# Optimization experiments

Hardware: AMD Instinct MI355X
Metric: run time of the kernel (lower is better)

## Reference

```python
import jax, jax.numpy as jnp
import numpy as np

B, S, H, NH = 2, 2048, 1024, 16
DK = H // NH

def setup_inputs() -> dict:
    key = jax.random.key(0)
    ks = jax.random.split(key, 8)
    scale = 0.02
    return {
        "x": jax.random.normal(ks[0], (B, S, H), jnp.float32),
        "mask": jax.random.randint(ks[1], (B, S, S), 0, 2, jnp.int32),
        "alibi": jax.random.normal(ks[2], (1, NH, S, S), jnp.float32),
        "W_q": jax.random.normal(ks[3], (H, H), jnp.float32) * scale,
        "b_q": jnp.zeros((H,), jnp.float32),
        "W_k": jax.random.normal(ks[4], (H, H), jnp.float32) * scale,
        "b_k": jnp.zeros((H,), jnp.float32),
        "W_v": jax.random.normal(ks[5], (H, H), jnp.float32) * scale,
        "b_v": jnp.zeros((H,), jnp.float32),
        "W_o": jax.random.normal(ks[6], (H, H), jnp.float32) * scale,
        "b_o": jnp.zeros((H,), jnp.float32),
    }

def reference(x, mask, alibi, W_q, b_q, W_k, b_k, W_v, b_v, W_o, b_o):
    b, s, h = x.shape
    def split_heads(t):  # [B,S,H] -> [B,NH,S,DK]
        return t.reshape(b, s, NH, DK).transpose(0, 2, 1, 3)
    q = split_heads(x @ W_q + b_q)
    k = split_heads(x @ W_k + b_k)
    v = split_heads(x @ W_v + b_v)
    scores = jnp.einsum("bhqd,bhkd->bhqk", q, k) / jnp.sqrt(jnp.float32(DK))
    scores = scores + alibi
    scores = jnp.where(mask[:, None, :, :] == 0, jnp.float32(-1e9), scores)
    probs = jax.nn.softmax(scores, axis=-1)  # dropout is identity in eval
    ctx = jnp.einsum("bhqk,bhkd->bhqd", probs, v)
    ctx = ctx.transpose(0, 2, 1, 3).reshape(b, s, h)
    return ctx @ W_o + b_o
```

## Files before the change

kernel.cpp:

```cpp
#include <hip/hip_runtime.h>
#include <hip/hip_bf16.h>


#define S_LEN 2048
#define H_DIM 1024
#define N_HEADS 16

typedef __bf16 bf16x8 __attribute__((ext_vector_type(8)));
typedef __bf16 bf16x4 __attribute__((ext_vector_type(4)));
typedef float f32x4 __attribute__((ext_vector_type(4)));

using gvoid = __attribute__((address_space(1))) void;
using svoid = __attribute__((address_space(3))) void;

static __device__ __forceinline__ f32x4 mfma16(bf16x8 a, bf16x8 b, f32x4 c) {
  return __builtin_amdgcn_mfma_f32_16x16x32_bf16(a, b, c, 0, 0, 0);
}

template <int NCH, int NW>
static __device__ __forceinline__ void stage64(const __bf16* g, int rstride,
                                               __bf16* lds, int wid, int lane) {
#pragma unroll
  for (int i = 0; i < NCH / NW; ++i) {
    int chunk = i * NW + wid;
    int u = chunk * 64 + lane;
    int r = u >> 3, s = u & 7;
    const __bf16* src = g + (size_t)r * rstride + ((s ^ (r & 7)) << 3);
    __builtin_amdgcn_global_load_lds((const gvoid*)src,
                                     (svoid*)(lds + chunk * 512), 16, 0, 0);
  }
}

static __device__ __forceinline__ bf16x8 read_frag(const __bf16* lds, int r,
                                                   int slot) {
  return *(const bf16x8*)(lds + r * 64 + ((slot ^ (r & 7)) << 3));
}

__global__ __launch_bounds__(256) void k_convert_x(const float* __restrict__ x,
                                                   __bf16* __restrict__ xb) {
  size_t idx = ((size_t)blockIdx.x * 256 + threadIdx.x) * 8;
  float4 a = *(const float4*)(x + idx);
  float4 b = *(const float4*)(x + idx + 4);
  bf16x8 o;
  o[0] = (__bf16)a.x; o[1] = (__bf16)a.y; o[2] = (__bf16)a.z; o[3] = (__bf16)a.w;
  o[4] = (__bf16)b.x; o[5] = (__bf16)b.y; o[6] = (__bf16)b.z; o[7] = (__bf16)b.w;
  *(bf16x8*)(xb + idx) = o;
}

__global__ __launch_bounds__(256) void k_transpose_w(
    const float* __restrict__ w0, const float* __restrict__ w1,
    const float* __restrict__ w2, const float* __restrict__ w3,
    __bf16* __restrict__ wt) {
  __shared__ float t[64][65];
  int z = blockIdx.z;
  const float* W = (z == 0) ? w0 : (z == 1) ? w1 : (z == 2) ? w2 : w3;
  __bf16* O = wt + (size_t)z * H_DIM * H_DIM;
  int k0 = blockIdx.x * 64, n0 = blockIdx.y * 64;
  int tid = threadIdx.x;
  {
    int r = tid >> 4, c4 = tid & 15;
#pragma unroll
    for (int i = 0; i < 4; ++i) {
      float4 v = *(const float4*)(W + (size_t)(k0 + r + i * 16) * H_DIM + n0 + c4 * 4);
      t[r + i * 16][c4 * 4 + 0] = v.x;
      t[r + i * 16][c4 * 4 + 1] = v.y;
      t[r + i * 16][c4 * 4 + 2] = v.z;
      t[r + i * 16][c4 * 4 + 3] = v.w;
    }
  }
  __syncthreads();
  {
    int nn = tid >> 2, js = (tid & 3) * 16;
    bf16x8 o0, o1;
#pragma unroll
    for (int j = 0; j < 8; ++j) {
      o0[j] = (__bf16)t[js + j][nn];
      o1[j] = (__bf16)t[js + 8 + j][nn];
    }
    __bf16* dst = O + (size_t)(n0 + nn) * H_DIM + k0 + js;
    *(bf16x8*)dst = o0;
    *(bf16x8*)(dst + 8) = o1;
  }
}

__global__ __launch_bounds__(256) void k_transpose_v(const __bf16* __restrict__ V,
                                                     __bf16* __restrict__ VT) {
  __shared__ __bf16 t[64][65];
  int bh = blockIdx.y;
  int s0 = blockIdx.x * 64;
  const __bf16* Vb = V + (size_t)bh * S_LEN * 64;
  int tid = threadIdx.x;
#pragma unroll
  for (int i = 0; i < 2; ++i) {
    int u = i * 256 + tid;
    int r = u >> 3, c8 = u & 7;
    bf16x8 v = *(const bf16x8*)(Vb + (size_t)(s0 + r) * 64 + c8 * 8);
#pragma unroll
    for (int j = 0; j < 8; ++j) t[r][c8 * 8 + j] = v[j];
  }
  __syncthreads();
  int d = tid >> 2, js = (tid & 3) * 16;
  bf16x8 o0, o1;
#pragma unroll
  for (int j = 0; j < 8; ++j) {
    o0[j] = t[js + j][d];
    o1[j] = t[js + 8 + j][d];
  }
  __bf16* dst = VT + (size_t)bh * 64 * S_LEN + (size_t)d * S_LEN + s0 + js;
  *(bf16x8*)dst = o0;
  *(bf16x8*)(dst + 8) = o1;
}

__global__ __launch_bounds__(256) void k_pack_mask(
    const int* __restrict__ m, unsigned long long* __restrict__ out) {
  size_t idx = (size_t)blockIdx.x * 256 + threadIdx.x;
  unsigned long long b = __ballot(m[idx] != 0);
  if ((threadIdx.x & 63) == 0) out[idx >> 6] = b;
}

template <int MODE>
__global__ __launch_bounds__(256) void k_gemm(
    const __bf16* __restrict__ A, const __bf16* __restrict__ B0,
    const __bf16* __restrict__ B1, const __bf16* __restrict__ B2,
    const float* __restrict__ bias0, const float* __restrict__ bias1,
    const float* __restrict__ bias2, __bf16* __restrict__ O0,
    __bf16* __restrict__ O1, __bf16* __restrict__ O2, float* __restrict__ Of) {
  __shared__ alignas(16) __bf16 As[128 * 64];
  __shared__ alignas(16) __bf16 Bs[128 * 64];
  int tid = threadIdx.x, wid = tid >> 6, lane = tid & 63;
  int l15 = lane & 15, lg = lane >> 4;
  int nbase = blockIdx.x * 128, mbase = blockIdx.y * 128;
  const __bf16* Bm;
  const float* bias;
  __bf16* Ob;
  float oscale = 1.0f;
  if (MODE == 0) {
    int z = blockIdx.z;
    Bm = (z == 0) ? B0 : (z == 1) ? B1 : B2;
    bias = (z == 0) ? bias0 : (z == 1) ? bias1 : bias2;
    Ob = (z == 0) ? O0 : (z == 1) ? O1 : O2;
    if (z == 0) oscale = 0.125f;
  } else {
    Bm = B0; bias = bias0; Ob = O0;
  }
  int wrow = wid >> 1, wcol = wid & 1;
  f32x4 zero = {0.f, 0.f, 0.f, 0.f};
  f32x4 acc[4][4];
#pragma unroll
  for (int i = 0; i < 4; ++i)
#pragma unroll
    for (int j = 0; j < 4; ++j) acc[i][j] = zero;

  for (int kb = 0; kb < H_DIM; kb += 64) {
    __syncthreads();
    const __bf16* Abase;
    int arstride;
    if (MODE == 0) {
      Abase = A + (size_t)mbase * H_DIM + kb;
      arstride = H_DIM;
    } else {
      int b = mbase >> 11, q0 = mbase & 2047, head = kb >> 6;
      Abase = A + ((size_t)(b * N_HEADS + head) * S_LEN + q0) * 64;
      arstride = 64;
    }
    stage64<16, 4>(Abase, arstride, As, wid, lane);
    stage64<16, 4>(Bm + (size_t)nbase * H_DIM + kb, H_DIM, Bs, wid, lane);
    __syncthreads();
#pragma unroll
    for (int t = 0; t < 2; ++t) {
      bf16x8 a[4], bfr[4];
#pragma unroll
      for (int i = 0; i < 4; ++i)
        a[i] = read_frag(As, wrow * 64 + i * 16 + l15, t * 4 + lg);
#pragma unroll
      for (int j = 0; j < 4; ++j)
        bfr[j] = read_frag(Bs, wcol * 64 + j * 16 + l15, t * 4 + lg);
#pragma unroll
      for (int i = 0; i < 4; ++i)
#pragma unroll
        for (int j = 0; j < 4; ++j) acc[i][j] = mfma16(a[i], bfr[j], acc[i][j]);
    }
  }
  float bv[4];
#pragma unroll
  for (int j = 0; j < 4; ++j) bv[j] = bias[nbase + wcol * 64 + j * 16 + l15];
#pragma unroll
  for (int i = 0; i < 4; ++i)
#pragma unroll
    for (int j = 0; j < 4; ++j)
#pragma unroll
      for (int r = 0; r < 4; ++r) {
        int m = mbase + wrow * 64 + i * 16 + lg * 4 + r;
        int col = nbase + wcol * 64 + j * 16 + l15;
        float v = (acc[i][j][r] + bv[j]) * oscale;
        if (MODE == 0) {
          size_t off =
              (((size_t)(m >> 11) * N_HEADS + (col >> 6)) * S_LEN + (m & 2047)) * 64 +
              (col & 63);
          Ob[off] = (__bf16)v;
        } else {
          Of[(size_t)m * H_DIM + col] = v;
        }
      }
}

__global__ __launch_bounds__(512) void k_attn(
    const __bf16* __restrict__ Q, const __bf16* __restrict__ K,
    const __bf16* __restrict__ VT, const float* __restrict__ alibi,
    const unsigned long long* __restrict__ maskb, __bf16* __restrict__ ctx) {
  __shared__ alignas(16) __bf16 Ks[2][64 * 64];
  __shared__ alignas(16) __bf16 Vs[64 * 64];
  __shared__ alignas(16) __bf16 Ps[8][16 * 72];
  int tid = threadIdx.x, wid = tid >> 6, lane = tid & 63;
  int l15 = lane & 15, lg = lane >> 4;
  int bh = blockIdx.x;
  int b = bh & 1, h = bh >> 1;
  int qbase = blockIdx.y * 128;
  size_t bho = (size_t)(b * N_HEADS + h);
  const __bf16* Qb = Q + bho * S_LEN * 64;
  const __bf16* Kb = K + bho * S_LEN * 64;
  const __bf16* Vb = VT + bho * 64 * S_LEN;
  const int q = qbase + wid * 16 + l15;

  bf16x8 qa[2];
  {
    const __bf16* qrow = Qb + (size_t)q * 64;
    qa[0] = *(const bf16x8*)(qrow + lg * 8);
    qa[1] = *(const bf16x8*)(qrow + 32 + lg * 8);
  }
  float mrun = -__builtin_inff(), lrun = 0.f;
  f32x4 cacc[4];
  f32x4 zero = {0.f, 0.f, 0.f, 0.f};
#pragma unroll
  for (int c = 0; c < 4; ++c) cacc[c] = zero;

  const float* arow = alibi + ((size_t)h * S_LEN + q) * S_LEN + lg * 4;
  const unsigned long long* mrow = maskb + ((size_t)b * S_LEN + q) * (S_LEN / 64);

  stage64<8, 8>(Kb, 64, Ks[0], wid, lane);
  __builtin_amdgcn_sched_barrier(0);
  f32x4 albP[4];
  unsigned long long mskP;
#pragma unroll
  for (int c = 0; c < 4; ++c) albP[c] = *(const f32x4*)(arow + c * 16);
  mskP = mrow[0];
  __builtin_amdgcn_sched_barrier(0);

  for (int t = 0; t < S_LEN / 64; ++t) {
    const int cur = t & 1;
    asm volatile("s_waitcnt vmcnt(5)" ::: "memory");
    __builtin_amdgcn_sched_barrier(0);
    __builtin_amdgcn_s_barrier();
    __builtin_amdgcn_sched_barrier(0);
    stage64<8, 8>(Vb + (size_t)t * 64, S_LEN, Vs, wid, lane);
    __builtin_amdgcn_sched_barrier(0);
    const int kn = (t < S_LEN / 64 - 1 ? t + 1 : t) * 64;
    stage64<8, 8>(Kb + (size_t)kn * 64, 64, Ks[cur ^ 1], wid, lane);
    __builtin_amdgcn_sched_barrier(0);

    f32x4 sacc[4];
#pragma unroll
    for (int c = 0; c < 4; ++c) sacc[c] = zero;
#pragma unroll
    for (int t2 = 0; t2 < 2; ++t2) {
      bf16x8 kf[4];
#pragma unroll
      for (int c = 0; c < 4; ++c)
        kf[c] = read_frag(Ks[cur], c * 16 + l15, t2 * 4 + lg);
#pragma unroll
      for (int c = 0; c < 4; ++c) sacc[c] = mfma16(kf[c], qa[t2], sacc[c]);
    }

    unsigned long long sh = mskP >> (lg * 4);
    float s[4][4];
    float m16 = -__builtin_inff();
#pragma unroll
    for (int c = 0; c < 4; ++c) {
      unsigned bits = (unsigned)(sh >> (c * 16)) & 0xFu;
#pragma unroll
      for (int r = 0; r < 4; ++r) {
        float a = (bits & (1u << r)) ? albP[c][r] : -1e9f;
        float v = sacc[c][r] + a;
        s[c][r] = v;
        m16 = fmaxf(m16, v);
      }
    }
    m16 = fmaxf(m16, __shfl_xor(m16, 16));
    m16 = fmaxf(m16, __shfl_xor(m16, 32));
    const bool norsc = __all(m16 <= mrun);
    float mn = fmaxf(mrun, m16);
    float scl = __expf(mrun - mn);
    mrun = mn;
    float rs = 0.f;
#pragma unroll
    for (int c = 0; c < 4; ++c)
#pragma unroll
      for (int r = 0; r < 4; ++r) {
        float pe = __expf(s[c][r] - mn);
        s[c][r] = pe;
        rs += pe;
      }
    rs += __shfl_xor(rs, 16);
    rs += __shfl_xor(rs, 32);
    lrun = lrun * scl + rs;
    if (!norsc) {
#pragma unroll
      for (int c = 0; c < 4; ++c) {
        f32x4 v = cacc[c];
        v[0] *= scl; v[1] *= scl; v[2] *= scl; v[3] *= scl;
        cacc[c] = v;
      }
    }
#pragma unroll
    for (int c = 0; c < 4; ++c) {
      bf16x4 u;
#pragma unroll
      for (int r = 0; r < 4; ++r) u[r] = (__bf16)s[c][r];
      *(bf16x4*)(&Ps[wid][l15 * 72 + c * 16 + lg * 4]) = u;
    }
    __builtin_amdgcn_sched_barrier(0);
#pragma unroll
    for (int c = 0; c < 4; ++c) albP[c] = *(const f32x4*)(arow + kn + c * 16);
    mskP = mrow[kn >> 6];
    __builtin_amdgcn_sched_barrier(0);
    asm volatile("s_waitcnt vmcnt(6)" ::: "memory");
    __builtin_amdgcn_sched_barrier(0);
    __builtin_amdgcn_s_barrier();
    __builtin_amdgcn_sched_barrier(0);
#pragma unroll
    for (int t2 = 0; t2 < 2; ++t2) {
      bf16x8 pa = *(const bf16x8*)(&Ps[wid][l15 * 72 + t2 * 32 + lg * 8]);
#pragma unroll
      for (int c = 0; c < 4; ++c) {
        bf16x8 vb = read_frag(Vs, c * 16 + l15, t2 * 4 + lg);
        cacc[c] = mfma16(vb, pa, cacc[c]);
      }
    }
  }
  float inv = 1.0f / lrun;
#pragma unroll
  for (int c = 0; c < 4; ++c) {
    bf16x4 u;
#pragma unroll
    for (int r = 0; r < 4; ++r) u[r] = (__bf16)(cacc[c][r] * inv);
    *(bf16x4*)(ctx + bho * S_LEN * 64 + (size_t)q * 64 + c * 16 + lg * 4) = u;
  }
}

extern "C" void kernel_launch(void* const* d_in, const int* in_sizes, int n_in,
                              void* d_out, int out_size, void* d_ws,
                              size_t ws_size, hipStream_t stream) {
  const float* x = (const float*)d_in[0];
  const int* mask = (const int*)d_in[1];
  const float* alibi = (const float*)d_in[2];
  const float* Wq = (const float*)d_in[3];
  const float* bq = (const float*)d_in[4];
  const float* Wk = (const float*)d_in[5];
  const float* bk = (const float*)d_in[6];
  const float* Wv = (const float*)d_in[7];
  const float* bv = (const float*)d_in[8];
  const float* Wo = (const float*)d_in[9];
  const float* bo = (const float*)d_in[10];
  float* out = (float*)d_out;
  char* ws = (char*)d_ws;

  const size_t MB = 1u << 20;
  __bf16* xb = (__bf16*)(ws);
  __bf16* wt = (__bf16*)(ws + 8 * MB);
  __bf16* Qb = (__bf16*)(ws + 16 * MB);
  __bf16* Kb = (__bf16*)(ws + 24 * MB);
  __bf16* Vb = (__bf16*)(ws + 32 * MB);
  __bf16* VTb = (__bf16*)(ws + 40 * MB);
  __bf16* ctxb = xb;
  __bf16* wtq = wt;
  __bf16* wtk = wt + (1u << 20);
  __bf16* wtv = wt + 2 * (1u << 20);
  __bf16* wto = wt + 3 * (1u << 20);
  unsigned long long* maskb = (unsigned long long*)Vb;

  k_convert_x<<<dim3(2048), 256, 0, stream>>>(x, xb);
  k_transpose_w<<<dim3(16, 16, 4), 256, 0, stream>>>(Wq, Wk, Wv, Wo, wt);
  k_gemm<0><<<dim3(8, 32, 3), 256, 0, stream>>>(xb, wtq, wtk, wtv, bq, bk, bv,
                                                Qb, Kb, Vb, nullptr);
  k_transpose_v<<<dim3(32, 32), 256, 0, stream>>>(Vb, VTb);
  k_pack_mask<<<dim3((2 * S_LEN * S_LEN) / 256), 256, 0, stream>>>(mask, maskb);
  k_attn<<<dim3(32, 16), 512, 0, stream>>>(Qb, Kb, VTb, alibi, maskb, ctxb);
  k_gemm<1><<<dim3(8, 32, 1), 256, 0, stream>>>(ctxb, wto, nullptr, nullptr, bo,
                                                nullptr, nullptr, nullptr,
                                                nullptr, nullptr, out);
}
```

Before: 239.2 us.

## Split attention over key halves with 1024-thread blocks and combine partials

The attention kernel now splits the key range into two halves across grid z, with 1024-thread blocks handling 256 queries. K and V staging is split between wave groups, and V is double-buffered. Alibi is preloaded into the MFMA accumulator, and s_setprio is placed around the MFMA sections. Partial outputs and their (max, sum) pairs go to fp32 workspace, and a new combine kernel merges them into bf16 ctx. This adds an extra kernel launch and fp32 partial traffic. It also removes the vmcnt waits that guarded the next tile's alibi and mask loads, so load ordering relies on the remaining waits.

Result: slower. 496.6 us (+107.6%).

```diff
diff --git a/kernel.cpp b/kernel.cpp
--- a/kernel.cpp
+++ b/kernel.cpp
@@ -9,6 +9,7 @@
 typedef __bf16 bf16x8 __attribute__((ext_vector_type(8)));
 typedef __bf16 bf16x4 __attribute__((ext_vector_type(4)));
 typedef float f32x4 __attribute__((ext_vector_type(4)));
+typedef unsigned long long u64;
 
 using gvoid = __attribute__((address_space(1))) void;
 using svoid = __attribute__((address_space(3))) void;
@@ -29,6 +30,15 @@
     __builtin_amdgcn_global_load_lds((const gvoid*)src,
                                      (svoid*)(lds + chunk * 512), 16, 0, 0);
   }
+}
+
+static __device__ __forceinline__ void stage1(const __bf16* g, int rstride,
+                                              __bf16* lds, int chunk, int lane) {
+  int u = chunk * 64 + lane;
+  int r = u >> 3, s = u & 7;
+  const __bf16* src = g + (size_t)r * rstride + ((s ^ (r & 7)) << 3);
+  __builtin_amdgcn_global_load_lds((const gvoid*)src,
+                                   (svoid*)(lds + chunk * 512), 16, 0, 0);
 }
 
 static __device__ __forceinline__ bf16x8 read_frag(const __bf16* lds, int r,
@@ -111,10 +121,10 @@
   *(bf16x8*)(dst + 8) = o1;
 }
 
-__global__ __launch_bounds__(256) void k_pack_mask(
-    const int* __restrict__ m, unsigned long long* __restrict__ out) {
+__global__ __launch_bounds__(256) void k_pack_mask(const int* __restrict__ m,
+                                                   u64* __restrict__ out) {
   size_t idx = (size_t)blockIdx.x * 256 + threadIdx.x;
-  unsigned long long b = __ballot(m[idx] != 0);
+  u64 b = __ballot(m[idx] != 0);
   if ((threadIdx.x & 63) == 0) out[idx >> 6] = b;
 }
 
@@ -204,23 +214,29 @@
       }
 }
 
-__global__ __launch_bounds__(512) void k_attn(
+__global__ __launch_bounds__(1024, 8) void k_attn(
     const __bf16* __restrict__ Q, const __bf16* __restrict__ K,
     const __bf16* __restrict__ VT, const float* __restrict__ alibi,
-    const unsigned long long* __restrict__ maskb, __bf16* __restrict__ ctx) {
+    const u64* __restrict__ maskb, float* __restrict__ Op,
+    float* __restrict__ ml) {
   __shared__ alignas(16) __bf16 Ks[2][64 * 64];
-  __shared__ alignas(16) __bf16 Vs[64 * 64];
-  __shared__ alignas(16) __bf16 Ps[8][16 * 72];
+  __shared__ alignas(16) __bf16 Vs[2][64 * 64];
+  __shared__ alignas(16) __bf16 Ps[16][16 * 72];
   int tid = threadIdx.x, wid = tid >> 6, lane = tid & 63;
   int l15 = lane & 15, lg = lane >> 4;
   int bh = blockIdx.x;
   int b = bh & 1, h = bh >> 1;
-  int qbase = blockIdx.y * 128;
+  int qbase = blockIdx.y * 256;
+  int z = blockIdx.z;
   size_t bho = (size_t)(b * N_HEADS + h);
   const __bf16* Qb = Q + bho * S_LEN * 64;
-  const __bf16* Kb = K + bho * S_LEN * 64;
-  const __bf16* Vb = VT + bho * 64 * S_LEN;
+  const __bf16* Kbz = K + (bho * S_LEN + (size_t)z * 1024) * 64;
+  const __bf16* Vbz = VT + bho * 64 * S_LEN + z * 1024;
   const int q = qbase + wid * 16 + l15;
+
+  const bool kduty = wid < 8;
+  const int chunk = kduty ? wid : wid - 8;
+  const int gstride = kduty ? 64 : S_LEN;
 
   bf16x8 qa[2];
   {
@@ -234,33 +250,34 @@
 #pragma unroll
   for (int c = 0; c < 4; ++c) cacc[c] = zero;
 
-  const float* arow = alibi + ((size_t)h * S_LEN + q) * S_LEN + lg * 4;
-  const unsigned long long* mrow = maskb + ((size_t)b * S_LEN + q) * (S_LEN / 64);
-
-  stage64<8, 8>(Kb, 64, Ks[0], wid, lane);
+  const float* arowz = alibi + ((size_t)h * S_LEN + q) * S_LEN + z * 1024 + lg * 4;
+  const u64* mrowz = maskb + ((size_t)b * S_LEN + q) * (S_LEN / 64) + z * 16;
+
+  const int NT = 16;
+  stage1(kduty ? Kbz : Vbz, gstride, kduty ? Ks[0] : Vs[0], chunk, lane);
   __builtin_amdgcn_sched_barrier(0);
   f32x4 albP[4];
-  unsigned long long mskP;
-#pragma unroll
-  for (int c = 0; c < 4; ++c) albP[c] = *(const f32x4*)(arow + c * 16);
-  mskP = mrow[0];
+  u64 mskP;
+#pragma unroll
+  for (int c = 0; c < 4; ++c) albP[c] = *(const f32x4*)(arowz + c * 16);
+  mskP = mrowz[0];
   __builtin_amdgcn_sched_barrier(0);
 
-  for (int t = 0; t < S_LEN / 64; ++t) {
+  for (int t = 0; t < NT; ++t) {
     const int cur = t & 1;
     asm volatile("s_waitcnt vmcnt(5)" ::: "memory");
     __builtin_amdgcn_sched_barrier(0);
     __builtin_amdgcn_s_barrier();
     __builtin_amdgcn_sched_barrier(0);
-    stage64<8, 8>(Vb + (size_t)t * 64, S_LEN, Vs, wid, lane);
+    const int tn = (t + 1 < NT) ? t + 1 : t;
+    stage1(kduty ? (Kbz + (size_t)tn * 64 * 64) : (Vbz + tn * 64), gstride,
+           kduty ? Ks[cur ^ 1] : Vs[cur ^ 1], chunk, lane);
     __builtin_amdgcn_sched_barrier(0);
-    const int kn = (t < S_LEN / 64 - 1 ? t + 1 : t) * 64;
-    stage64<8, 8>(Kb + (size_t)kn * 64, 64, Ks[cur ^ 1], wid, lane);
-    __builtin_amdgcn_sched_barrier(0);
 
     f32x4 sacc[4];
 #pragma unroll
-    for (int c = 0; c < 4; ++c) sacc[c] = zero;
+    for (int c = 0; c < 4; ++c) sacc[c] = albP[c];
+    __builtin_amdgcn_s_setprio(1);
 #pragma unroll
     for (int t2 = 0; t2 < 2; ++t2) {
       bf16x8 kf[4];
@@ -270,8 +287,13 @@
 #pragma unroll
       for (int c = 0; c < 4; ++c) sacc[c] = mfma16(kf[c], qa[t2], sacc[c]);
     }
-
-    unsigned long long sh = mskP >> (lg * 4);
+    __builtin_amdgcn_s_setprio(0);
+    u64 sh = mskP >> (lg * 4);
+#pragma unroll
+    for (int c = 0; c < 4; ++c)
+      albP[c] = *(const f32x4*)(arowz + tn * 64 + c * 16);
+    mskP = mrowz[tn];
+
     float s[4][4];
     float m16 = -__builtin_inff();
 #pragma unroll
@@ -279,8 +301,7 @@
       unsigned bits = (unsigned)(sh >> (c * 16)) & 0xFu;
 #pragma unroll
       for (int r = 0; r < 4; ++r) {
-        float a = (bits & (1u << r)) ? albP[c][r] : -1e9f;
-        float v = sacc[c][r] + a;
+        float v = (bits & (1u << r)) ? sacc[c][r] : -1e9f;
         s[c][r] = v;
         m16 = fmaxf(m16, v);
       }
@@ -319,32 +340,46 @@
       *(bf16x4*)(&Ps[wid][l15 * 72 + c * 16 + lg * 4]) = u;
     }
     __builtin_amdgcn_sched_barrier(0);
-#pragma unroll
-    for (int c = 0; c < 4; ++c) albP[c] = *(const f32x4*)(arow + kn + c * 16);
-    mskP = mrow[kn >> 6];
-    __builtin_amdgcn_sched_barrier(0);
-    asm volatile("s_waitcnt vmcnt(6)" ::: "memory");
-    __builtin_amdgcn_sched_barrier(0);
     __builtin_amdgcn_s_barrier();
     __builtin_amdgcn_sched_barrier(0);
+    __builtin_amdgcn_s_setprio(1);
 #pragma unroll
     for (int t2 = 0; t2 < 2; ++t2) {
       bf16x8 pa = *(const bf16x8*)(&Ps[wid][l15 * 72 + t2 * 32 + lg * 8]);
 #pragma unroll
       for (int c = 0; c < 4; ++c) {
-        bf16x8 vb = read_frag(Vs, c * 16 + l15, t2 * 4 + lg);
+        bf16x8 vb = read_frag(Vs[cur], c * 16 + l15, t2 * 4 + lg);
         cacc[c] = mfma16(vb, pa, cacc[c]);
       }
     }
-  }
-  float inv = 1.0f / lrun;
-#pragma unroll
-  for (int c = 0; c < 4; ++c) {
-    bf16x4 u;
-#pragma unroll
-    for (int r = 0; r < 4; ++r) u[r] = (__bf16)(cacc[c][r] * inv);
-    *(bf16x4*)(ctx + bho * S_LEN * 64 + (size_t)q * 64 + c * 16 + lg * 4) = u;
-  }
+    __builtin_amdgcn_s_setprio(0);
+  }
+  asm volatile("s_waitcnt vmcnt(0)" ::: "memory");
+  float* op = Op + (((size_t)z * 32 + bho) * S_LEN + q) * 64;
+#pragma unroll
+  for (int c = 0; c < 4; ++c) *(f32x4*)(op + c * 16 + lg * 4) = cacc[c];
+  if (lg == 0) {
+    float2* mlp = (float2*)(ml + (((size_t)z * 32 + bho) * S_LEN + q) * 2);
+    *mlp = make_float2(mrun, lrun);
+  }
+}
+
+__global__ __launch_bounds__(256) void k_combine(const float* __restrict__ Op,
+                                                 const float* __restrict__ ml,
+                                                 __bf16* __restrict__ ctx) {
+  int t = blockIdx.x * 256 + threadIdx.x;
+  int dgrp = t & 15, qq = t >> 4;
+  float2 m0 = *(const float2*)(ml + (size_t)qq * 2);
+  float2 m1 = *(const float2*)(ml + ((size_t)65536 + qq) * 2);
+  float m = fmaxf(m0.x, m1.x);
+  float e0 = __expf(m0.x - m), e1 = __expf(m1.x - m);
+  float inv = 1.f / (m0.y * e0 + m1.y * e1);
+  f32x4 a = *(const f32x4*)(Op + (size_t)qq * 64 + dgrp * 4);
+  f32x4 c = *(const f32x4*)(Op + (size_t)65536 * 64 + (size_t)qq * 64 + dgrp * 4);
+  bf16x4 o;
+#pragma unroll
+  for (int j = 0; j < 4; ++j) o[j] = (__bf16)((a[j] * e0 + c[j] * e1) * inv);
+  *(bf16x4*)(ctx + (size_t)qq * 64 + dgrp * 4) = o;
 }
 
 extern "C" void kernel_launch(void* const* d_in, const int* in_sizes, int n_in,
@@ -371,12 +406,14 @@
   __bf16* Kb = (__bf16*)(ws + 24 * MB);
   __bf16* Vb = (__bf16*)(ws + 32 * MB);
   __bf16* VTb = (__bf16*)(ws + 40 * MB);
+  float* Op = (float*)(ws + 48 * MB);
+  float* mlb = (float*)(ws + 80 * MB);
   __bf16* ctxb = xb;
   __bf16* wtq = wt;
   __bf16* wtk = wt + (1u << 20);
   __bf16* wtv = wt + 2 * (1u << 20);
   __bf16* wto = wt + 3 * (1u << 20);
-  unsigned long long* maskb = (unsigned long long*)Vb;
+  u64* maskb = (u64*)Vb;
 
   k_convert_x<<<dim3(2048), 256, 0, stream>>>(x, xb);
   k_transpose_w<<<dim3(16, 16, 4), 256, 0, stream>>>(Wq, Wk, Wv, Wo, wt);
@@ -384,7 +421,9 @@
                                                 Qb, Kb, Vb, nullptr);
   k_transpose_v<<<dim3(32, 32), 256, 0, stream>>>(Vb, VTb);
   k_pack_mask<<<dim3((2 * S_LEN * S_LEN) / 256), 256, 0, stream>>>(mask, maskb);
-  k_attn<<<dim3(32, 16), 512, 0, stream>>>(Qb, Kb, VTb, alibi, maskb, ctxb);
+  k_attn<<<dim3(32, 8, 2), 1024, 0, stream>>>(Qb, Kb, VTb, alibi, maskb, Op,
+                                              mlb);
+  k_combine<<<dim3(4096), 256, 0, stream>>>(Op, mlb, ctxb);
   k_gemm<1><<<dim3(8, 32, 1), 256, 0, stream>>>(ctxb, wto, nullptr, nullptr, bo,
                                                 nullptr, nullptr, nullptr,
                                                 nullptr, nullptr, out);
```

## Fuse V transpose into QKV GEMM epilogue and preload alibi into score accumulator

Applied to the files above, without the earlier changes.

The QKV GEMM epilogue now writes V directly in transposed [d, s] layout with 4-wide bf16 stores, removing the separate V transpose kernel and its round trip through memory. In attention, the alibi values initialise the QK^T accumulator so the MFMA adds them for free, and the next tile's alibi and mask loads are issued earlier, right after the score MFMAs. s_setprio raises wave priority around the MFMA sections. The mask buffer gets its own workspace region. The risks are different vmcnt accounting and narrow strided stores in the V epilogue.

Measured after the change: 238.4 us. Within noise of the previous version (-0.3%).

```diff
diff --git a/kernel.cpp b/kernel.cpp
--- a/kernel.cpp
+++ b/kernel.cpp
@@ -9,6 +9,7 @@
 typedef __bf16 bf16x8 __attribute__((ext_vector_type(8)));
 typedef __bf16 bf16x4 __attribute__((ext_vector_type(4)));
 typedef float f32x4 __attribute__((ext_vector_type(4)));
+typedef unsigned long long u64;
 
 using gvoid = __attribute__((address_space(1))) void;
 using svoid = __attribute__((address_space(3))) void;
@@ -83,38 +84,10 @@
   }
 }
 
-__global__ __launch_bounds__(256) void k_transpose_v(const __bf16* __restrict__ V,
-                                                     __bf16* __restrict__ VT) {
-  __shared__ __bf16 t[64][65];
-  int bh = blockIdx.y;
-  int s0 = blockIdx.x * 64;
-  const __bf16* Vb = V + (size_t)bh * S_LEN * 64;
-  int tid = threadIdx.x;
-#pragma unroll
-  for (int i = 0; i < 2; ++i) {
-    int u = i * 256 + tid;
-    int r = u >> 3, c8 = u & 7;
-    bf16x8 v = *(const bf16x8*)(Vb + (size_t)(s0 + r) * 64 + c8 * 8);
-#pragma unroll
-    for (int j = 0; j < 8; ++j) t[r][c8 * 8 + j] = v[j];
-  }
-  __syncthreads();
-  int d = tid >> 2, js = (tid & 3) * 16;
-  bf16x8 o0, o1;
-#pragma unroll
-  for (int j = 0; j < 8; ++j) {
-    o0[j] = t[js + j][d];
-    o1[j] = t[js + 8 + j][d];
-  }
-  __bf16* dst = VT + (size_t)bh * 64 * S_LEN + (size_t)d * S_LEN + s0 + js;
-  *(bf16x8*)dst = o0;
-  *(bf16x8*)(dst + 8) = o1;
-}
-
-__global__ __launch_bounds__(256) void k_pack_mask(
-    const int* __restrict__ m, unsigned long long* __restrict__ out) {
+__global__ __launch_bounds__(256) void k_pack_mask(const int* __restrict__ m,
+                                                   u64* __restrict__ out) {
   size_t idx = (size_t)blockIdx.x * 256 + threadIdx.x;
-  unsigned long long b = __ballot(m[idx] != 0);
+  u64 b = __ballot(m[idx] != 0);
   if ((threadIdx.x & 63) == 0) out[idx >> 6] = b;
 }
 
@@ -134,12 +107,12 @@
   const float* bias;
   __bf16* Ob;
   float oscale = 1.0f;
+  const int zv = (MODE == 0) ? blockIdx.z : 0;
   if (MODE == 0) {
-    int z = blockIdx.z;
-    Bm = (z == 0) ? B0 : (z == 1) ? B1 : B2;
-    bias = (z == 0) ? bias0 : (z == 1) ? bias1 : bias2;
-    Ob = (z == 0) ? O0 : (z == 1) ? O1 : O2;
-    if (z == 0) oscale = 0.125f;
+    Bm = (zv == 0) ? B0 : (zv == 1) ? B1 : B2;
+    bias = (zv == 0) ? bias0 : (zv == 1) ? bias1 : bias2;
+    Ob = (zv == 0) ? O0 : (zv == 1) ? O1 : O2;
+    if (zv == 0) oscale = 0.125f;
   } else {
     Bm = B0; bias = bias0; Ob = O0;
   }
@@ -187,27 +160,43 @@
 #pragma unroll
   for (int i = 0; i < 4; ++i)
 #pragma unroll
-    for (int j = 0; j < 4; ++j)
-#pragma unroll
-      for (int r = 0; r < 4; ++r) {
-        int m = mbase + wrow * 64 + i * 16 + lg * 4 + r;
+    for (int j = 0; j < 4; ++j) {
+      if (MODE == 0 && zv == 2) {
+        int m0 = mbase + wrow * 64 + i * 16 + lg * 4;
         int col = nbase + wcol * 64 + j * 16 + l15;
-        float v = (acc[i][j][r] + bv[j]) * oscale;
-        if (MODE == 0) {
-          size_t off =
-              (((size_t)(m >> 11) * N_HEADS + (col >> 6)) * S_LEN + (m & 2047)) * 64 +
-              (col & 63);
-          Ob[off] = (__bf16)v;
-        } else {
-          Of[(size_t)m * H_DIM + col] = v;
+        bf16x4 u;
+#pragma unroll
+        for (int r = 0; r < 4; ++r) u[r] = (__bf16)(acc[i][j][r] + bv[j]);
+        size_t off =
+            (((size_t)(m0 >> 11) * N_HEADS + (col >> 6)) * 64 + (col & 63)) *
+                (size_t)S_LEN +
+            (m0 & 2047);
+        *(bf16x4*)(Ob + off) = u;
+      } else {
+#pragma unroll
+        for (int r = 0; r < 4; ++r) {
+          int m = mbase + wrow * 64 + i * 16 + lg * 4 + r;
+          int col = nbase + wcol * 64 + j * 16 + l15;
+          float v = (acc[i][j][r] + bv[j]) * oscale;
+          if (MODE == 0) {
+            size_t off =
+                (((size_t)(m >> 11) * N_HEADS + (col >> 6)) * S_LEN +
+                 (m & 2047)) *
+                    64 +
+                (col & 63);
+            Ob[off] = (__bf16)v;
+          } else {
+            Of[(size_t)m * H_DIM + col] = v;
+          }
         }
       }
+    }
 }
 
 __global__ __launch_bounds__(512) void k_attn(
     const __bf16* __restrict__ Q, const __bf16* __restrict__ K,
     const __bf16* __restrict__ VT, const float* __restrict__ alibi,
-    const unsigned long long* __restrict__ maskb, __bf16* __restrict__ ctx) {
+    const u64* __restrict__ maskb, __bf16* __restrict__ ctx) {
   __shared__ alignas(16) __bf16 Ks[2][64 * 64];
   __shared__ alignas(16) __bf16 Vs[64 * 64];
   __shared__ alignas(16) __bf16 Ps[8][16 * 72];
@@ -235,12 +224,12 @@
   for (int c = 0; c < 4; ++c) cacc[c] = zero;
 
   const float* arow = alibi + ((size_t)h * S_LEN + q) * S_LEN + lg * 4;
-  const unsigned long long* mrow = maskb + ((size_t)b * S_LEN + q) * (S_LEN / 64);
+  const u64* mrow = maskb + ((size_t)b * S_LEN + q) * (S_LEN / 64);
 
   stage64<8, 8>(Kb, 64, Ks[0], wid, lane);
   __builtin_amdgcn_sched_barrier(0);
   f32x4 albP[4];
-  unsigned long long mskP;
+  u64 mskP;
 #pragma unroll
   for (int c = 0; c < 4; ++c) albP[c] = *(const f32x4*)(arow + c * 16);
   mskP = mrow[0];
@@ -252,15 +241,16 @@
     __builtin_amdgcn_sched_barrier(0);
     __builtin_amdgcn_s_barrier();
     __builtin_amdgcn_sched_barrier(0);
-    stage64<8, 8>(Vb + (size_t)t * 64, S_LEN, Vs, wid, lane);
-    __builtin_amdgcn_sched_barrier(0);
-    const int kn = (t < S_LEN / 64 - 1 ? t + 1 : t) * 64;
-    stage64<8, 8>(Kb + (size_t)kn * 64, 64, Ks[cur ^ 1], wid, lane);
+    stage64<8, 8>(Vb + t * 64, S_LEN, Vs, wid, lane);
+    __builtin_amdgcn_sched_barrier(0);
+    const int tn = (t + 1 < S_LEN / 64) ? t + 1 : t;
+    stage64<8, 8>(Kb + (size_t)tn * 64 * 64, 64, Ks[cur ^ 1], wid, lane);
     __builtin_amdgcn_sched_barrier(0);
 
     f32x4 sacc[4];
 #pragma unroll
-    for (int c = 0; c < 4; ++c) sacc[c] = zero;
+    for (int c = 0; c < 4; ++c) sacc[c] = albP[c];
+    __builtin_amdgcn_s_setprio(1);
 #pragma unroll
     for (int t2 = 0; t2 < 2; ++t2) {
       bf16x8 kf[4];
@@ -270,8 +260,13 @@
 #pragma unroll
       for (int c = 0; c < 4; ++c) sacc[c] = mfma16(kf[c], qa[t2], sacc[c]);
     }
-
-    unsigned long long sh = mskP >> (lg * 4);
+    __builtin_amdgcn_s_setprio(0);
+    u64 sh = mskP >> (lg * 4);
+#pragma unroll
+    for (int c = 0; c < 4; ++c)
+      albP[c] = *(const f32x4*)(arow + tn * 64 + c * 16);
+    mskP = mrow[tn];
+
     float s[4][4];
     float m16 = -__builtin_inff();
 #pragma unroll
@@ -279,8 +274,7 @@
       unsigned bits = (unsigned)(sh >> (c * 16)) & 0xFu;
 #pragma unroll
       for (int r = 0; r < 4; ++r) {
-        float a = (bits & (1u << r)) ? albP[c][r] : -1e9f;
-        float v = sacc[c][r] + a;
+        float v = (bits & (1u << r)) ? sacc[c][r] : -1e9f;
         s[c][r] = v;
         m16 = fmaxf(m16, v);
       }
@@ -319,14 +313,11 @@
       *(bf16x4*)(&Ps[wid][l15 * 72 + c * 16 + lg * 4]) = u;
     }
     __builtin_amdgcn_sched_barrier(0);
-#pragma unroll
-    for (int c = 0; c < 4; ++c) albP[c] = *(const f32x4*)(arow + kn + c * 16);
-    mskP = mrow[kn >> 6];
-    __builtin_amdgcn_sched_barrier(0);
     asm volatile("s_waitcnt vmcnt(6)" ::: "memory");
     __builtin_amdgcn_sched_barrier(0);
     __builtin_amdgcn_s_barrier();
     __builtin_amdgcn_sched_barrier(0);
+    __builtin_amdgcn_s_setprio(1);
 #pragma unroll
     for (int t2 = 0; t2 < 2; ++t2) {
       bf16x8 pa = *(const bf16x8*)(&Ps[wid][l15 * 72 + t2 * 32 + lg * 8]);
@@ -336,7 +327,9 @@
         cacc[c] = mfma16(vb, pa, cacc[c]);
       }
     }
-  }
+    __builtin_amdgcn_s_setprio(0);
+  }
+  asm volatile("s_waitcnt vmcnt(0)" ::: "memory");
   float inv = 1.0f / lrun;
 #pragma unroll
   for (int c = 0; c < 4; ++c) {
@@ -369,20 +362,18 @@
   __bf16* wt = (__bf16*)(ws + 8 * MB);
   __bf16* Qb = (__bf16*)(ws + 16 * MB);
   __bf16* Kb = (__bf16*)(ws + 24 * MB);
-  __bf16* Vb = (__bf16*)(ws + 32 * MB);
-  __bf16* VTb = (__bf16*)(ws + 40 * MB);
+  __bf16* VTb = (__bf16*)(ws + 32 * MB);
+  u64* maskb = (u64*)(ws + 40 * MB);
   __bf16* ctxb = xb;
   __bf16* wtq = wt;
   __bf16* wtk = wt + (1u << 20);
   __bf16* wtv = wt + 2 * (1u << 20);
   __bf16* wto = wt + 3 * (1u << 20);
-  unsigned long long* maskb = (unsigned long long*)Vb;
 
   k_convert_x<<<dim3(2048), 256, 0, stream>>>(x, xb);
   k_transpose_w<<<dim3(16, 16, 4), 256, 0, stream>>>(Wq, Wk, Wv, Wo, wt);
   k_gemm<0><<<dim3(8, 32, 3), 256, 0, stream>>>(xb, wtq, wtk, wtv, bq, bk, bv,
-                                                Qb, Kb, Vb, nullptr);
-  k_transpose_v<<<dim3(32, 32), 256, 0, stream>>>(Vb, VTb);
+                                                Qb, Kb, VTb, nullptr);
   k_pack_mask<<<dim3((2 * S_LEN * S_LEN) / 256), 256, 0, stream>>>(mask, maskb);
   k_attn<<<dim3(32, 16), 512, 0, stream>>>(Qb, Kb, VTb, alibi, maskb, ctxb);
   k_gemm<1><<<dim3(8, 32, 1), 256, 0, stream>>>(ctxb, wto, nullptr, nullptr, bo,
```
